# Performance work log

Measured on AMD Instinct MI355X. Metric: run time of the kernel, lower is better.

## Reference

```python
import jax, jax.numpy as jnp
import numpy as np

N_NODES = 50000
N_EDGES = 1_600_000
IN_FEAT = 64
HIDDEN = 64
OUT_FEAT = 10
NUM_LAYERS = 8
ALPHA = 0.1
THETA = 0.5
LN_EPS = 1e-5


def setup_inputs() -> dict:
    key = jax.random.key(0)
    ks = jax.random.split(key, 6)
    N, E, Fin, H, C = N_NODES, N_EDGES, IN_FEAT, HIDDEN, OUT_FEAT
    return {
        "x": jax.random.normal(ks[0], (N, Fin), jnp.float32),
        "W_lin": jax.random.normal(ks[1], (Fin, H), jnp.float32) / np.float32(np.sqrt(Fin)),
        "b_lin": jnp.zeros((H,), jnp.float32),
        "Ws": jax.random.normal(ks[2], (NUM_LAYERS, H, H), jnp.float32) / np.float32(np.sqrt(H)),
        "W1": jax.random.normal(ks[3], (2 * H, H), jnp.float32) / np.float32(np.sqrt(2 * H)),
        "b1": jnp.zeros((H,), jnp.float32),
        "ln_g": jnp.ones((H,), jnp.float32),
        "ln_b": jnp.zeros((H,), jnp.float32),
        "W2": jax.random.normal(ks[4], (H, C), jnp.float32) / np.float32(np.sqrt(H)),
        "b2": jnp.zeros((C,), jnp.float32),
        "edge_index": jax.random.randint(ks[5], (2, E), 0, N, jnp.int32),
    }


def _gcn_norm(edge_index, n):
    # PyG gcn_norm: add self-loops, symmetric D^-1/2 A D^-1/2 normalization.
    loop = jnp.arange(n, dtype=edge_index.dtype)
    row = jnp.concatenate([edge_index[0], loop])
    col = jnp.concatenate([edge_index[1], loop])
    w = jnp.ones(row.shape[0], jnp.float32)
    deg = jax.ops.segment_sum(w, col, num_segments=n)
    dinv = jnp.where(deg > 0, jax.lax.rsqrt(deg), 0.0)
    return row, col, dinv[row] * dinv[col]


def reference(x, W_lin, b_lin, Ws, W1, b1, ln_g, ln_b, W2, b2, edge_index):
    n = x.shape[0]
    row, col, vals = _gcn_norm(edge_index, n)
    h = jax.nn.relu(x @ W_lin + b_lin)  # [N, H]
    h0 = h
    for layer in range(NUM_LAYERS):
        beta = np.float32(np.log(THETA / (layer + 1) + 1.0))
        # SpMM: out[i] = sum over edges (i<-j) vals * h[j]
        agg = jax.ops.segment_sum(vals[:, None] * h[col], row, num_segments=n)
        mix = (1.0 - ALPHA) * agg + ALPHA * h0  # GCN2 initial-residual
        h = jax.nn.relu((1.0 - beta) * mix + beta * (mix @ Ws[layer]))  # identity mapping
    # mix_node_features 'cat': gather endpoint features per edge -> [E, 2H]
    line_x = jnp.concatenate([h[edge_index[0]], h[edge_index[1]]], axis=-1)
    # ClassifierMLP2: Linear -> LayerNorm -> ReLU -> Linear
    z = line_x @ W1 + b1
    mu = jnp.mean(z, axis=-1, keepdims=True)
    var = jnp.var(z, axis=-1, keepdims=True)
    z = (z - mu) * jax.lax.rsqrt(var + LN_EPS) * ln_g + ln_b
    z = jax.nn.relu(z)
    return z @ W2 + b2  # [E, out_features]
```

## Files before the change

kernel.cpp:

```cpp
#include <hip/hip_runtime.h>
#include <hip/hip_fp16.h>
#include <math.h>

#define N_NODES 50000
#define N_EDGES 1600000
#define EDGE_GRID 2048
#define ESTRIDE (EDGE_GRID*64)
#define CAP 128

#define NB 64
#define BRANGE 782
#define BCAP 28672
#define BIN_BLOCKS 512
#define EPB (N_EDGES/BIN_BLOCKS)
#define CURPAD 32

using half8  = __attribute__((ext_vector_type(8))) _Float16;
using half4  = __attribute__((ext_vector_type(4))) _Float16;
using float4v = __attribute__((ext_vector_type(4))) float;

__device__ __forceinline__ float rl(float v, int srclane){
  return __int_as_float(__builtin_amdgcn_readlane(__float_as_int(v), srclane));
}

__global__ __launch_bounds__(256) void k_bin(const int* __restrict__ rowE, const int* __restrict__ colE,
                                             unsigned* __restrict__ rstream, unsigned short* __restrict__ cstream,
                                             int* __restrict__ rcur, int* __restrict__ ccur){
  __shared__ int hr[NB], hc[NB], br[NB], bc[NB];
  int t = threadIdx.x;
  if(t < NB){ hr[t] = 0; hc[t] = 0; }
  __syncthreads();
  int e0 = blockIdx.x * EPB;
  for(int e = e0 + t; e < e0 + EPB; e += 256){
    int r = __builtin_nontemporal_load(rowE + e);
    int c = __builtin_nontemporal_load(colE + e);
    atomicAdd(&hr[r/BRANGE], 1);
    atomicAdd(&hc[c/BRANGE], 1);
  }
  __syncthreads();
  if(t < NB){
    br[t] = atomicAdd(&rcur[t*CURPAD], hr[t]); hr[t] = 0;
    bc[t] = atomicAdd(&ccur[t*CURPAD], hc[t]); hc[t] = 0;
  }
  __syncthreads();
  for(int e = e0 + t; e < e0 + EPB; e += 256){
    int r = rowE[e];
    int c = colE[e];
    int rb = r/BRANGE, cb = c/BRANGE;
    int rp = br[rb] + atomicAdd(&hr[rb], 1);
    int cp = bc[cb] + atomicAdd(&hc[cb], 1);
    if(rp < BCAP) rstream[(size_t)rb*BCAP + rp] = ((unsigned)r << 16) | (unsigned)c;
    if(cp < BCAP) cstream[(size_t)cb*BCAP + cp] = (unsigned short)c;
  }
}

__global__ __launch_bounds__(256) void k_build(const unsigned* __restrict__ rstream,
                                               const unsigned short* __restrict__ cstream,
                                               const int* __restrict__ rcur, const int* __restrict__ ccur,
                                               int* __restrict__ row_fill, int* __restrict__ degcnt,
                                               unsigned short* __restrict__ csr_col){
  __shared__ int lf[BRANGE];
  int b = blockIdx.x & (NB-1);
  int role = blockIdx.x >> 6;
  int base = b*BRANGE;
  int range = min(BRANGE, N_NODES - base);
  int t = threadIdx.x;
  for(int i=t;i<range;i+=256) lf[i] = 0;
  __syncthreads();
  if(role == 0){
    int cnt = min(rcur[b*CURPAD], BCAP);
    const unsigned* sp = rstream + (size_t)b*BCAP;
    for(int i=t;i<cnt;i+=256){
      unsigned rc = sp[i];
      int r = (int)(rc >> 16), c = (int)(rc & 0xffffu);
      int pos = atomicAdd(&lf[r-base], 1);
      if(pos < CAP) csr_col[(size_t)r*CAP + pos] = (unsigned short)c;
    }
    __syncthreads();
    for(int i=t;i<range;i+=256) row_fill[base+i] = lf[i];
  } else {
    int cnt = min(ccur[b*CURPAD], BCAP);
    const unsigned short* sp = cstream + (size_t)b*BCAP;
    for(int i=t;i<cnt;i+=256){
      int c = (int)sp[i];
      atomicAdd(&lf[c-base], 1);
    }
    __syncthreads();
    for(int i=t;i<range;i+=256) degcnt[base+i] = lf[i];
  }
}

__global__ void k_dinv(int* __restrict__ degcnt_rdeg, float* __restrict__ dinv,
                       __half* __restrict__ gA, __half* __restrict__ gB){
  int i = blockIdx.x*256 + threadIdx.x;
  if(i < N_NODES){
    float dp1 = (float)(degcnt_rdeg[i] + 1);
    dinv[i] = rsqrtf(dp1);
    ((float*)degcnt_rdeg)[i] = sqrtf(dp1);
  }
  if(i < 64){
    gA[(size_t)N_NODES*64 + i] = __float2half(0.f);
    gB[(size_t)N_NODES*64 + i] = __float2half(0.f);
  }
}


__global__ __launch_bounds__(256) void k_lin0(const float* __restrict__ x, const float* __restrict__ W,
                                              const float* __restrict__ b, const float* __restrict__ dinv,
                                              __half* __restrict__ h0, __half* __restrict__ g0){
  __shared__ float Wl[4096];
  int t = threadIdx.x;
  for(int i=t;i<4096;i+=256) Wl[i] = W[i];
  __syncthreads();
  int wave = t>>6, lane = t&63;
  int row0 = blockIdx.x*16 + wave*4;
  float4 xq = ((const float4*)(x + (size_t)row0*64))[lane];
  float a0=0,a1=0,a2=0,a3=0;
  #pragma unroll
  for(int k=0;k<64;k++){
    float w = Wl[k*64+lane];
    float comp = ((k&3)==0)?xq.x:((k&3)==1)?xq.y:((k&3)==2)?xq.z:xq.w;
    a0 += rl(comp,      (k>>2)) * w;
    a1 += rl(comp, 16 + (k>>2)) * w;
    a2 += rl(comp, 32 + (k>>2)) * w;
    a3 += rl(comp, 48 + (k>>2)) * w;
  }
  float bb = b[lane];
  float h[4] = {fmaxf(a0+bb,0.f), fmaxf(a1+bb,0.f), fmaxf(a2+bb,0.f), fmaxf(a3+bb,0.f)};
  #pragma unroll
  for(int r=0;r<4;r++){
    float dv = dinv[row0+r];
    h0[(size_t)(row0+r)*64+lane] = __float2half(h[r]);
    g0[(size_t)(row0+r)*64+lane] = __float2half(dv*h[r]);
  }
}

__global__ __launch_bounds__(256) void k_ab(const __half* __restrict__ g, const float* __restrict__ rdeg,
                                            const float* __restrict__ W1,
                                            __half* __restrict__ A, __half* __restrict__ B){
  __shared__ float Wa[4096];
  __shared__ float Wb[4096];
  int t = threadIdx.x;
  for(int i=t;i<4096;i+=256){ Wa[i] = W1[i]; Wb[i] = W1[4096+i]; }
  __syncthreads();
  int wave = t>>6, lane = t&63;
  int row0 = blockIdx.x*16 + wave*4;
  int myrow = row0 + (lane>>4);
  float rd = rdeg[myrow];
  const __half2* hp = (const __half2*)(g + (size_t)row0*64);
  __half2 p01 = hp[2*lane], p23 = hp[2*lane+1];
  float2 f01 = __half22float2(p01), f23 = __half22float2(p23);
  float4 xq = make_float4(f01.x*rd, f01.y*rd, f23.x*rd, f23.y*rd);
  float a0=0,a1=0,a2=0,a3=0,b0=0,b1=0,b2=0,b3=0;
  #pragma unroll
  for(int k=0;k<64;k++){
    float wa = Wa[k*64+lane], wb = Wb[k*64+lane];
    float comp = ((k&3)==0)?xq.x:((k&3)==1)?xq.y:((k&3)==2)?xq.z:xq.w;
    float s0 = rl(comp,      (k>>2));
    float s1 = rl(comp, 16 + (k>>2));
    float s2 = rl(comp, 32 + (k>>2));
    float s3 = rl(comp, 48 + (k>>2));
    a0 += s0*wa; a1 += s1*wa; a2 += s2*wa; a3 += s3*wa;
    b0 += s0*wb; b1 += s1*wb; b2 += s2*wb; b3 += s3*wb;
  }
  A[(size_t)(row0+0)*64+lane]=__float2half(a0); A[(size_t)(row0+1)*64+lane]=__float2half(a1);
  A[(size_t)(row0+2)*64+lane]=__float2half(a2); A[(size_t)(row0+3)*64+lane]=__float2half(a3);
  B[(size_t)(row0+0)*64+lane]=__float2half(b0); B[(size_t)(row0+1)*64+lane]=__float2half(b1);
  B[(size_t)(row0+2)*64+lane]=__float2half(b2); B[(size_t)(row0+3)*64+lane]=__float2half(b3);
}

__global__ __launch_bounds__(256) void k_layer(const __half* __restrict__ g_in, const __half* __restrict__ h0,
                          const int* __restrict__ row_fill, const unsigned short* __restrict__ csr_col,
                          const float* __restrict__ dinv,
                          const float* __restrict__ Wsl, float beta, __half* __restrict__ g_out){
  __shared__ __align__(16) _Float16 tile[16*72];
  int t = threadIdx.x, wave = t>>6, lane = t&63;
  int quad = lane>>4, l15 = lane&15;

  half8 bfrag0, bfrag1;
  int n = 16*wave + l15;
  #pragma unroll
  for(int j=0;j<8;j++){
    int k0 = quad*8 + j;
    int k1 = 32 + quad*8 + j;
    float v0 = beta*Wsl[k0*64+n] + ((k0==n)?(1.f-beta):0.f);
    float v1 = beta*Wsl[k1*64+n] + ((k1==n)?(1.f-beta):0.f);
    bfrag0[j] = (_Float16)v0;
    bfrag1[j] = (_Float16)v1;
  }

  int i0 = blockIdx.x*16;
  int iw = i0 + 4*wave;

  int deg[4], cv[4];
  half4 selfv[4], h0v[4];
  float dv[4];
  #pragma unroll
  for(int r=0;r<4;r++) deg[r] = min(row_fill[iw+r], CAP);
  #pragma unroll
  for(int r=0;r<4;r++){
    const unsigned short* colp = csr_col + (size_t)(iw+r)*CAP;
    cv[r] = (lane < deg[r]) ? (int)__builtin_nontemporal_load(colp + lane) : 0;
  }
  #pragma unroll
  for(int r=0;r<4;r++){
    dv[r]    = dinv[iw+r];
    selfv[r] = *(const half4*)(g_in + (size_t)(iw+r)*64 + 4*l15);
    h0v[r]   = *(const half4*)(h0   + (size_t)(iw+r)*64 + 4*l15);
  }

  for(int r=0;r<4;r++){
    const unsigned short* colp = csr_col + (size_t)(iw+r)*CAP;
    float4v acc = {0.f,0.f,0.f,0.f};
    int base = 0;
    int cur  = cv[r];
    for(;;){
      int rem = deg[r] - base; if(rem > 64) rem = 64;
      int nit = (rem + 3) >> 2;
      int it = 0;
      for(; it+4<=nit; it+=4){
        int i0x = 4*it + quad, i1x = i0x+4, i2x = i0x+8, i3x = i0x+12;
        int c0 = __shfl(cur, i0x, 64); c0 = (i0x < rem) ? c0 : N_NODES;
        int c1 = __shfl(cur, i1x, 64); c1 = (i1x < rem) ? c1 : N_NODES;
        int c2 = __shfl(cur, i2x, 64); c2 = (i2x < rem) ? c2 : N_NODES;
        int c3 = __shfl(cur, i3x, 64); c3 = (i3x < rem) ? c3 : N_NODES;
        half4 v0 = *(const half4*)(g_in + (size_t)c0*64 + 4*l15);
        half4 v1 = *(const half4*)(g_in + (size_t)c1*64 + 4*l15);
        half4 v2 = *(const half4*)(g_in + (size_t)c2*64 + 4*l15);
        half4 v3 = *(const half4*)(g_in + (size_t)c3*64 + 4*l15);
        #pragma unroll
        for(int k=0;k<4;k++) acc[k] += ((float)v0[k]+(float)v1[k]) + ((float)v2[k]+(float)v3[k]);
      }
      for(; it+2<=nit; it+=2){
        int i0x = 4*it + quad, i1x = i0x+4;
        int c0 = __shfl(cur, i0x, 64); c0 = (i0x < rem) ? c0 : N_NODES;
        int c1 = __shfl(cur, i1x, 64); c1 = (i1x < rem) ? c1 : N_NODES;
        half4 v0 = *(const half4*)(g_in + (size_t)c0*64 + 4*l15);
        half4 v1 = *(const half4*)(g_in + (size_t)c1*64 + 4*l15);
        #pragma unroll
        for(int k=0;k<4;k++) acc[k] += (float)v0[k] + (float)v1[k];
      }
      if(it < nit){
        int i0x = 4*it + quad;
        int c0 = __shfl(cur, i0x, 64); c0 = (i0x < rem) ? c0 : N_NODES;
        half4 v0 = *(const half4*)(g_in + (size_t)c0*64 + 4*l15);
        #pragma unroll
        for(int k=0;k<4;k++) acc[k] += (float)v0[k];
      }
      base += 64;
      if(base >= deg[r]) break;
      cur = (base + lane < deg[r]) ? (int)__builtin_nontemporal_load(colp + base + lane) : 0;
    }
    #pragma unroll
    for(int k=0;k<4;k++){
      acc[k] += __shfl_xor(acc[k], 16, 64);
      acc[k] += __shfl_xor(acc[k], 32, 64);
    }
    if(quad == 0){
      half4 mixv;
      #pragma unroll
      for(int k=0;k<4;k++){
        float m = 0.9f*dv[r]*(acc[k] + (float)selfv[r][k]) + 0.1f*(float)h0v[r][k];
        mixv[k] = (_Float16)m;
      }
      *(half4*)&tile[(4*wave+r)*72 + 4*l15] = mixv;
    }
  }
  __syncthreads();

  float4v acc4 = {0.f,0.f,0.f,0.f};
  half8 afrag0 = *(const half8*)&tile[l15*72 + quad*8];
  half8 afrag1 = *(const half8*)&tile[l15*72 + quad*8 + 32];
  acc4 = __builtin_amdgcn_mfma_f32_16x16x32_f16(afrag0, bfrag0, acc4, 0,0,0);
  acc4 = __builtin_amdgcn_mfma_f32_16x16x32_f16(afrag1, bfrag1, acc4, 0,0,0);
  #pragma unroll
  for(int r=0;r<4;r++){
    int row = quad*4 + r;
    float dvo = dinv[i0+row];
    g_out[(size_t)(i0+row)*64 + n] = __float2half(dvo*fmaxf(acc4[r], 0.f));
  }
}

__global__ __launch_bounds__(256) void k_edge(const __half* __restrict__ A, const __half* __restrict__ B,
                         const int* __restrict__ srcE, const int* __restrict__ dstE,
                         const float* __restrict__ b1v, const float* __restrict__ lng,
                         const float* __restrict__ lnb, const float* __restrict__ W2,
                         const float* __restrict__ b2v, float* __restrict__ out){
  int t = threadIdx.x, wave = t>>6, lane = t&63;
  int l15 = lane&15, quad = lane>>4;

  half8 bf0, bf1;
  #pragma unroll
  for(int j=0;j<8;j++){
    float w0 = (l15<10) ? W2[(quad*8+j)*10 + l15]    : 0.f;
    float w1 = (l15<10) ? W2[(32+quad*8+j)*10 + l15] : 0.f;
    bf0[j] = (_Float16)w0;
    bf1[j] = (_Float16)w1;
  }
  float b1r0[8], b1r1[8], gr0[8], gr1[8], br0[8], br1[8];
  #pragma unroll
  for(int j=0;j<8;j++){
    b1r0[j] = b1v[quad*8+j];    b1r1[j] = b1v[32+quad*8+j];
    gr0[j]  = lng[quad*8+j];    gr1[j]  = lng[32+quad*8+j];
    br0[j]  = lnb[quad*8+j];    br1[j]  = lnb[32+quad*8+j];
  }
  float bias = (l15<10) ? b2v[l15] : 0.f;

  int eb0 = blockIdx.x*64 + wave*16;
  int sC = __builtin_nontemporal_load(srcE + eb0 + l15);
  int dC = __builtin_nontemporal_load(dstE + eb0 + l15);
  int sN = 0, dN = 0;
  if(eb0 + ESTRIDE < N_EDGES){
    sN = __builtin_nontemporal_load(srcE + eb0 + ESTRIDE + l15);
    dN = __builtin_nontemporal_load(dstE + eb0 + ESTRIDE + l15);
  }
  half8 A0 = *(const half8*)(A + (size_t)sC*64 + quad*8);
  half8 A1 = *(const half8*)(A + (size_t)sC*64 + 32 + quad*8);
  half8 G0 = *(const half8*)(B + (size_t)dC*64 + quad*8);
  half8 G1 = *(const half8*)(B + (size_t)dC*64 + 32 + quad*8);

  for(int eb = eb0; eb < N_EDGES; eb += ESTRIDE){
    int s2 = 0, d2 = 0;
    if(eb + 2*ESTRIDE < N_EDGES){
      s2 = __builtin_nontemporal_load(srcE + eb + 2*ESTRIDE + l15);
      d2 = __builtin_nontemporal_load(dstE + eb + 2*ESTRIDE + l15);
    }
    half8 nA0 = *(const half8*)(A + (size_t)sN*64 + quad*8);
    half8 nA1 = *(const half8*)(A + (size_t)sN*64 + 32 + quad*8);
    half8 nG0 = *(const half8*)(B + (size_t)dN*64 + quad*8);
    half8 nG1 = *(const half8*)(B + (size_t)dN*64 + 32 + quad*8);

    float z0[8], z1[8];
    float s1 = 0.f, s2acc = 0.f;
    #pragma unroll
    for(int j=0;j<8;j++){
      float za = (float)A0[j] + (float)G0[j] + b1r0[j];
      float zb = (float)A1[j] + (float)G1[j] + b1r1[j];
      z0[j]=za; z1[j]=zb;
      s1 += za + zb;
      s2acc += za*za + zb*zb;
    }
    s1 += __shfl_xor(s1,16,64); s1 += __shfl_xor(s1,32,64);
    s2acc += __shfl_xor(s2acc,16,64); s2acc += __shfl_xor(s2acc,32,64);
    float mu  = s1*(1.f/64.f);
    float var = s2acc*(1.f/64.f) - mu*mu;
    float rs  = rsqrtf(var + 1e-5f);
    half8 af0, af1;
    #pragma unroll
    for(int j=0;j<8;j++){
      af0[j] = (_Float16)fmaxf((z0[j]-mu)*rs*gr0[j] + br0[j], 0.f);
      af1[j] = (_Float16)fmaxf((z1[j]-mu)*rs*gr1[j] + br1[j], 0.f);
    }
    float4v acc = {0.f,0.f,0.f,0.f};
    acc = __builtin_amdgcn_mfma_f32_16x16x32_f16(af0, bf0, acc, 0,0,0);
    acc = __builtin_amdgcn_mfma_f32_16x16x32_f16(af1, bf1, acc, 0,0,0);
    if(l15 < 10){
      #pragma unroll
      for(int r=0;r<4;r++){
        __builtin_nontemporal_store(acc[r] + bias, &out[(size_t)(eb + quad*4 + r)*10 + l15]);
      }
    }
    A0=nA0; A1=nA1; G0=nG0; G1=nG1;
    sN=s2; dN=d2;
  }
}


extern "C" void kernel_launch(void* const* d_in, const int* in_sizes, int n_in,
                              void* d_out, int out_size, void* d_ws, size_t ws_size,
                              hipStream_t stream){
  const float* x     = (const float*)d_in[0];
  const float* W_lin = (const float*)d_in[1];
  const float* b_lin = (const float*)d_in[2];
  const float* Ws    = (const float*)d_in[3];
  const float* W1    = (const float*)d_in[4];
  const float* b1    = (const float*)d_in[5];
  const float* ln_g  = (const float*)d_in[6];
  const float* ln_b  = (const float*)d_in[7];
  const float* W2    = (const float*)d_in[8];
  const float* b2    = (const float*)d_in[9];
  const int*   eidx  = (const int*)d_in[10];
  const int*   rowE  = eidx;
  const int*   colE  = eidx + N_EDGES;
  float* out = (float*)d_out;

  char* ws = (char*)d_ws;
  size_t o = 0;
  auto alloc = [&](size_t bytes)->char*{ char* p = ws + o; o = (o + bytes + 255) & ~(size_t)255; return p; };
  int*   row_fill= (int*)  alloc((size_t)N_NODES*4);
  int*   degcnt  = (int*)  alloc((size_t)N_NODES*4);
  float* dinv    = (float*)alloc((size_t)N_NODES*4);
  unsigned short* csr_col = (unsigned short*)alloc((size_t)N_NODES*CAP*2);
  unsigned* rstream = (unsigned*)alloc((size_t)NB*BCAP*4);
  unsigned short* cstream = (unsigned short*)alloc((size_t)NB*BCAP*2);
  int*   rcur    = (int*)  alloc((size_t)NB*CURPAD*4);
  int*   ccur    = (int*)  alloc((size_t)NB*CURPAD*4);
  __half* h0     = (__half*)alloc((size_t)(N_NODES+1)*64*2);
  __half* gA     = (__half*)alloc((size_t)(N_NODES+1)*64*2);
  __half* gB     = (__half*)alloc((size_t)(N_NODES+1)*64*2);
  float* rdeg    = (float*)degcnt;

  hipMemsetAsync(rcur, 0, (size_t)NB*CURPAD*4, stream);
  hipMemsetAsync(ccur, 0, (size_t)NB*CURPAD*4, stream);

  k_bin  <<<BIN_BLOCKS, 256, 0, stream>>>(rowE, colE, rstream, cstream, rcur, ccur);
  k_build<<<2*NB, 256, 0, stream>>>(rstream, cstream, rcur, ccur, row_fill, degcnt, csr_col);
  k_dinv <<<(N_NODES+255)/256, 256, 0, stream>>>(degcnt, dinv, gA, gB);

  k_lin0<<<N_NODES/16, 256, 0, stream>>>(x, W_lin, b_lin, dinv, h0, gA);

  const __half* gin = gA;
  __half* bufs[2] = {gB, gA};
  for(int L=0; L<8; L++){
    float beta = logf(0.5f/(float)(L+1) + 1.0f);
    __half* gout = bufs[L&1];
    k_layer<<<(N_NODES+15)/16, 256, 0, stream>>>(gin, h0, row_fill, csr_col, dinv,
                                                 Ws + (size_t)L*4096, beta, gout);
    gin = gout;
  }
  __half* Abuf = gB;
  __half* Bbuf = h0;
  k_ab<<<N_NODES/16, 256, 0, stream>>>(gA, rdeg, W1, Abuf, Bbuf);
  k_edge<<<EDGE_GRID, 256, 0, stream>>>(Abuf, Bbuf, rowE, colE, b1, ln_g, ln_b, W2, b2, out);
}
```

Before: 503.9 us.

## Gather neighbor rows with 16-byte loads in SpMM and drop edge-kernel prefetch

The layer SpMM now has each lane gather 8 halves (16 bytes) per neighbor. Eight lanes cover one 64-wide row, so a wave processes 8 neighbors at a time instead of 4 with 8-byte loads, and one extra xor-shuffle stage completes the reduction. The edge classifier kernel drops its software-pipelined prefetch of the next indices and features and becomes a simple grid-stride loop. The gather change aims to cut load instruction count per byte; removing the prefetch may expose gather latency or may lower register pressure and raise occupancy.

```diff
diff --git a/kernel.cpp b/kernel.cpp
--- a/kernel.cpp
+++ b/kernel.cpp
@@ -5,7 +5,6 @@
 #define N_NODES 50000
 #define N_EDGES 1600000
 #define EDGE_GRID 2048
-#define ESTRIDE (EDGE_GRID*64)
 #define CAP 128
 
 #define NB 64
@@ -176,6 +175,7 @@
   __shared__ __align__(16) _Float16 tile[16*72];
   int t = threadIdx.x, wave = t>>6, lane = t&63;
   int quad = lane>>4, l15 = lane&15;
+  int grp = lane>>3, l8 = lane&7;
 
   half8 bfrag0, bfrag1;
   int n = 16*wave + l15;
@@ -193,7 +193,7 @@
   int iw = i0 + 4*wave;
 
   int deg[4], cv[4];
-  half4 selfv[4], h0v[4];
+  half8 selfv[4], h0v[4];
   float dv[4];
   #pragma unroll
   for(int r=0;r<4;r++) deg[r] = min(row_fill[iw+r], CAP);
@@ -205,65 +205,53 @@
   #pragma unroll
   for(int r=0;r<4;r++){
     dv[r]    = dinv[iw+r];
-    selfv[r] = *(const half4*)(g_in + (size_t)(iw+r)*64 + 4*l15);
-    h0v[r]   = *(const half4*)(h0   + (size_t)(iw+r)*64 + 4*l15);
+    selfv[r] = *(const half8*)(g_in + (size_t)(iw+r)*64 + 8*l8);
+    h0v[r]   = *(const half8*)(h0   + (size_t)(iw+r)*64 + 8*l8);
   }
 
   for(int r=0;r<4;r++){
     const unsigned short* colp = csr_col + (size_t)(iw+r)*CAP;
-    float4v acc = {0.f,0.f,0.f,0.f};
+    float acc[8] = {0,0,0,0,0,0,0,0};
     int base = 0;
     int cur  = cv[r];
     for(;;){
       int rem = deg[r] - base; if(rem > 64) rem = 64;
-      int nit = (rem + 3) >> 2;
+      int nit = (rem + 7) >> 3;
       int it = 0;
-      for(; it+4<=nit; it+=4){
-        int i0x = 4*it + quad, i1x = i0x+4, i2x = i0x+8, i3x = i0x+12;
-        int c0 = __shfl(cur, i0x, 64); c0 = (i0x < rem) ? c0 : N_NODES;
-        int c1 = __shfl(cur, i1x, 64); c1 = (i1x < rem) ? c1 : N_NODES;
-        int c2 = __shfl(cur, i2x, 64); c2 = (i2x < rem) ? c2 : N_NODES;
-        int c3 = __shfl(cur, i3x, 64); c3 = (i3x < rem) ? c3 : N_NODES;
-        half4 v0 = *(const half4*)(g_in + (size_t)c0*64 + 4*l15);
-        half4 v1 = *(const half4*)(g_in + (size_t)c1*64 + 4*l15);
-        half4 v2 = *(const half4*)(g_in + (size_t)c2*64 + 4*l15);
-        half4 v3 = *(const half4*)(g_in + (size_t)c3*64 + 4*l15);
+      for(; it+2<=nit; it+=2){
+        int iA = 8*it + grp, iB = iA + 8;
+        int cA = __shfl(cur, iA, 64); cA = (iA < rem) ? cA : N_NODES;
+        int cB = __shfl(cur, iB, 64); cB = (iB < rem) ? cB : N_NODES;
+        half8 vA = *(const half8*)(g_in + (size_t)cA*64 + 8*l8);
+        half8 vB = *(const half8*)(g_in + (size_t)cB*64 + 8*l8);
         #pragma unroll
-        for(int k=0;k<4;k++) acc[k] += ((float)v0[k]+(float)v1[k]) + ((float)v2[k]+(float)v3[k]);
-      }
-      for(; it+2<=nit; it+=2){
-        int i0x = 4*it + quad, i1x = i0x+4;
-        int c0 = __shfl(cur, i0x, 64); c0 = (i0x < rem) ? c0 : N_NODES;
-        int c1 = __shfl(cur, i1x, 64); c1 = (i1x < rem) ? c1 : N_NODES;
-        half4 v0 = *(const half4*)(g_in + (size_t)c0*64 + 4*l15);
-        half4 v1 = *(const half4*)(g_in + (size_t)c1*64 + 4*l15);
-        #pragma unroll
-        for(int k=0;k<4;k++) acc[k] += (float)v0[k] + (float)v1[k];
+        for(int k=0;k<8;k++) acc[k] += (float)vA[k] + (float)vB[k];
       }
       if(it < nit){
-        int i0x = 4*it + quad;
-        int c0 = __shfl(cur, i0x, 64); c0 = (i0x < rem) ? c0 : N_NODES;
-        half4 v0 = *(const half4*)(g_in + (size_t)c0*64 + 4*l15);
+        int iA = 8*it + grp;
+        int cA = __shfl(cur, iA, 64); cA = (iA < rem) ? cA : N_NODES;
+        half8 vA = *(const half8*)(g_in + (size_t)cA*64 + 8*l8);
         #pragma unroll
-        for(int k=0;k<4;k++) acc[k] += (float)v0[k];
+        for(int k=0;k<8;k++) acc[k] += (float)vA[k];
       }
       base += 64;
       if(base >= deg[r]) break;
       cur = (base + lane < deg[r]) ? (int)__builtin_nontemporal_load(colp + base + lane) : 0;
     }
     #pragma unroll
-    for(int k=0;k<4;k++){
+    for(int k=0;k<8;k++){
+      acc[k] += __shfl_xor(acc[k], 8, 64);
       acc[k] += __shfl_xor(acc[k], 16, 64);
       acc[k] += __shfl_xor(acc[k], 32, 64);
     }
-    if(quad == 0){
-      half4 mixv;
+    if(grp == 0){
+      half8 mixv;
       #pragma unroll
-      for(int k=0;k<4;k++){
+      for(int k=0;k<8;k++){
         float m = 0.9f*dv[r]*(acc[k] + (float)selfv[r][k]) + 0.1f*(float)h0v[r][k];
         mixv[k] = (_Float16)m;
       }
-      *(half4*)&tile[(4*wave+r)*72 + 4*l15] = mixv;
+      *(half8*)&tile[(4*wave+r)*72 + 8*l8] = mixv;
     }
   }
   __syncthreads();
@@ -306,44 +294,28 @@
   }
   float bias = (l15<10) ? b2v[l15] : 0.f;
 
-  int eb0 = blockIdx.x*64 + wave*16;
-  int sC = __builtin_nontemporal_load(srcE + eb0 + l15);
-  int dC = __builtin_nontemporal_load(dstE + eb0 + l15);
-  int sN = 0, dN = 0;
-  if(eb0 + ESTRIDE < N_EDGES){
-    sN = __builtin_nontemporal_load(srcE + eb0 + ESTRIDE + l15);
-    dN = __builtin_nontemporal_load(dstE + eb0 + ESTRIDE + l15);
-  }
-  half8 A0 = *(const half8*)(A + (size_t)sC*64 + quad*8);
-  half8 A1 = *(const half8*)(A + (size_t)sC*64 + 32 + quad*8);
-  half8 G0 = *(const half8*)(B + (size_t)dC*64 + quad*8);
-  half8 G1 = *(const half8*)(B + (size_t)dC*64 + 32 + quad*8);
-
-  for(int eb = eb0; eb < N_EDGES; eb += ESTRIDE){
-    int s2 = 0, d2 = 0;
-    if(eb + 2*ESTRIDE < N_EDGES){
-      s2 = __builtin_nontemporal_load(srcE + eb + 2*ESTRIDE + l15);
-      d2 = __builtin_nontemporal_load(dstE + eb + 2*ESTRIDE + l15);
-    }
-    half8 nA0 = *(const half8*)(A + (size_t)sN*64 + quad*8);
-    half8 nA1 = *(const half8*)(A + (size_t)sN*64 + 32 + quad*8);
-    half8 nG0 = *(const half8*)(B + (size_t)dN*64 + quad*8);
-    half8 nG1 = *(const half8*)(B + (size_t)dN*64 + 32 + quad*8);
-
+  for(int eb = blockIdx.x*64 + wave*16; eb < N_EDGES; eb += EDGE_GRID*64){
+    int e = eb + l15;
+    int s = __builtin_nontemporal_load(srcE + e);
+    int d = __builtin_nontemporal_load(dstE + e);
+    half8 a0 = *(const half8*)(A + (size_t)s*64 + quad*8);
+    half8 a1 = *(const half8*)(A + (size_t)s*64 + 32 + quad*8);
+    half8 g0 = *(const half8*)(B + (size_t)d*64 + quad*8);
+    half8 g1 = *(const half8*)(B + (size_t)d*64 + 32 + quad*8);
     float z0[8], z1[8];
-    float s1 = 0.f, s2acc = 0.f;
+    float s1 = 0.f, s2 = 0.f;
     #pragma unroll
     for(int j=0;j<8;j++){
-      float za = (float)A0[j] + (float)G0[j] + b1r0[j];
-      float zb = (float)A1[j] + (float)G1[j] + b1r1[j];
+      float za = (float)a0[j] + (float)g0[j] + b1r0[j];
+      float zb = (float)a1[j] + (float)g1[j] + b1r1[j];
       z0[j]=za; z1[j]=zb;
       s1 += za + zb;
-      s2acc += za*za + zb*zb;
+      s2 += za*za + zb*zb;
     }
     s1 += __shfl_xor(s1,16,64); s1 += __shfl_xor(s1,32,64);
-    s2acc += __shfl_xor(s2acc,16,64); s2acc += __shfl_xor(s2acc,32,64);
+    s2 += __shfl_xor(s2,16,64); s2 += __shfl_xor(s2,32,64);
     float mu  = s1*(1.f/64.f);
-    float var = s2acc*(1.f/64.f) - mu*mu;
+    float var = s2*(1.f/64.f) - mu*mu;
     float rs  = rsqrtf(var + 1e-5f);
     half8 af0, af1;
     #pragma unroll
@@ -360,8 +332,6 @@
         __builtin_nontemporal_store(acc[r] + bias, &out[(size_t)(eb + quad*4 + r)*10 + l15]);
       }
     }
-    A0=nA0; A1=nA1; G0=nG0; G1=nG1;
-    sN=s2; dN=d2;
   }
 }
 
```

Result: slower. 550.6 us (+9.3%).

## Process edges in row-bucketed order in edge kernel for gather locality

Applied to the files above, without the earlier changes.

The bin pass now stores the original edge index alongside row/col in a 64-bit record. The final edge kernel walks these row-bucketed records instead of the raw edge list, so source-row gathers stay within one node range and hit cache better. Output is scattered back using the stored edge id. The cost is wider stream records, scattered output stores, and dropping the software prefetch pipeline from the old loop.

```diff
diff --git a/kernel.cpp b/kernel.cpp
--- a/kernel.cpp
+++ b/kernel.cpp
@@ -5,7 +5,6 @@
 #define N_NODES 50000
 #define N_EDGES 1600000
 #define EDGE_GRID 2048
-#define ESTRIDE (EDGE_GRID*64)
 #define CAP 128
 
 #define NB 64
@@ -24,7 +23,8 @@
 }
 
 __global__ __launch_bounds__(256) void k_bin(const int* __restrict__ rowE, const int* __restrict__ colE,
-                                             unsigned* __restrict__ rstream, unsigned short* __restrict__ cstream,
+                                             unsigned long long* __restrict__ rstream,
+                                             unsigned short* __restrict__ cstream,
                                              int* __restrict__ rcur, int* __restrict__ ccur){
   __shared__ int hr[NB], hc[NB], br[NB], bc[NB];
   int t = threadIdx.x;
@@ -49,12 +49,13 @@
     int rb = r/BRANGE, cb = c/BRANGE;
     int rp = br[rb] + atomicAdd(&hr[rb], 1);
     int cp = bc[cb] + atomicAdd(&hc[cb], 1);
-    if(rp < BCAP) rstream[(size_t)rb*BCAP + rp] = ((unsigned)r << 16) | (unsigned)c;
+    if(rp < BCAP) rstream[(size_t)rb*BCAP + rp] =
+        ((unsigned long long)(unsigned)e << 32) | ((unsigned)r << 16) | (unsigned)c;
     if(cp < BCAP) cstream[(size_t)cb*BCAP + cp] = (unsigned short)c;
   }
 }
 
-__global__ __launch_bounds__(256) void k_build(const unsigned* __restrict__ rstream,
+__global__ __launch_bounds__(256) void k_build(const unsigned long long* __restrict__ rstream,
                                                const unsigned short* __restrict__ cstream,
                                                const int* __restrict__ rcur, const int* __restrict__ ccur,
                                                int* __restrict__ row_fill, int* __restrict__ degcnt,
@@ -69,10 +70,10 @@
   __syncthreads();
   if(role == 0){
     int cnt = min(rcur[b*CURPAD], BCAP);
-    const unsigned* sp = rstream + (size_t)b*BCAP;
+    const unsigned long long* sp = rstream + (size_t)b*BCAP;
     for(int i=t;i<cnt;i+=256){
-      unsigned rc = sp[i];
-      int r = (int)(rc >> 16), c = (int)(rc & 0xffffu);
+      unsigned long long rec = sp[i];
+      int r = (int)((rec >> 16) & 0xffffu), c = (int)(rec & 0xffffu);
       int pos = atomicAdd(&lf[r-base], 1);
       if(pos < CAP) csr_col[(size_t)r*CAP + pos] = (unsigned short)c;
     }
@@ -183,10 +184,8 @@
   for(int j=0;j<8;j++){
     int k0 = quad*8 + j;
     int k1 = 32 + quad*8 + j;
-    float v0 = beta*Wsl[k0*64+n] + ((k0==n)?(1.f-beta):0.f);
-    float v1 = beta*Wsl[k1*64+n] + ((k1==n)?(1.f-beta):0.f);
-    bfrag0[j] = (_Float16)v0;
-    bfrag1[j] = (_Float16)v1;
+    bfrag0[j] = (_Float16)(beta*Wsl[k0*64+n] + ((k0==n)?(1.f-beta):0.f));
+    bfrag1[j] = (_Float16)(beta*Wsl[k1*64+n] + ((k1==n)?(1.f-beta):0.f));
   }
 
   int i0 = blockIdx.x*16;
@@ -282,7 +281,7 @@
 }
 
 __global__ __launch_bounds__(256) void k_edge(const __half* __restrict__ A, const __half* __restrict__ B,
-                         const int* __restrict__ srcE, const int* __restrict__ dstE,
+                         const unsigned long long* __restrict__ rstream, const int* __restrict__ rcur,
                          const float* __restrict__ b1v, const float* __restrict__ lng,
                          const float* __restrict__ lnb, const float* __restrict__ W2,
                          const float* __restrict__ b2v, float* __restrict__ out){
@@ -306,44 +305,39 @@
   }
   float bias = (l15<10) ? b2v[l15] : 0.f;
 
-  int eb0 = blockIdx.x*64 + wave*16;
-  int sC = __builtin_nontemporal_load(srcE + eb0 + l15);
-  int dC = __builtin_nontemporal_load(dstE + eb0 + l15);
-  int sN = 0, dN = 0;
-  if(eb0 + ESTRIDE < N_EDGES){
-    sN = __builtin_nontemporal_load(srcE + eb0 + ESTRIDE + l15);
-    dN = __builtin_nontemporal_load(dstE + eb0 + ESTRIDE + l15);
-  }
-  half8 A0 = *(const half8*)(A + (size_t)sC*64 + quad*8);
-  half8 A1 = *(const half8*)(A + (size_t)sC*64 + 32 + quad*8);
-  half8 G0 = *(const half8*)(B + (size_t)dC*64 + quad*8);
-  half8 G1 = *(const half8*)(B + (size_t)dC*64 + 32 + quad*8);
-
-  for(int eb = eb0; eb < N_EDGES; eb += ESTRIDE){
-    int s2 = 0, d2 = 0;
-    if(eb + 2*ESTRIDE < N_EDGES){
-      s2 = __builtin_nontemporal_load(srcE + eb + 2*ESTRIDE + l15);
-      d2 = __builtin_nontemporal_load(dstE + eb + 2*ESTRIDE + l15);
-    }
-    half8 nA0 = *(const half8*)(A + (size_t)sN*64 + quad*8);
-    half8 nA1 = *(const half8*)(A + (size_t)sN*64 + 32 + quad*8);
-    half8 nG0 = *(const half8*)(B + (size_t)dN*64 + quad*8);
-    half8 nG1 = *(const half8*)(B + (size_t)dN*64 + 32 + quad*8);
-
+  int bid = blockIdx.x;
+  int bucket = ((bid & 7) << 3) | ((bid >> 3) & 7);
+  int sub = bid >> 6;
+  int cnt = rcur[bucket*CURPAD]; if(cnt > BCAP) cnt = BCAP;
+  const unsigned long long* sp = rstream + (size_t)bucket*BCAP;
+  int chunk = ((cnt + 2047) >> 11) << 6;
+  int start = sub*chunk;
+  int end = start + chunk; if(end > cnt) end = cnt;
+
+  for(int eo = start + wave*16; eo < end; eo += 64){
+    int idx = eo + l15; if(idx >= end) idx = end - 1;
+    unsigned long long rec = sp[idx];
+    int s = (int)((rec >> 16) & 0xffffu);
+    int d = (int)(rec & 0xffffu);
+    int e = (int)(rec >> 32);
+    half8 a0 = *(const half8*)(A + (size_t)s*64 + quad*8);
+    half8 a1 = *(const half8*)(A + (size_t)s*64 + 32 + quad*8);
+    half8 g0 = *(const half8*)(B + (size_t)d*64 + quad*8);
+    half8 g1 = *(const half8*)(B + (size_t)d*64 + 32 + quad*8);
     float z0[8], z1[8];
-    float s1 = 0.f, s2acc = 0.f;
+    float s1 = 0.f, s2 = 0.f;
     #pragma unroll
     for(int j=0;j<8;j++){
-      float za = (float)A0[j] + (float)G0[j] + b1r0[j];
-      float zb = (float)A1[j] + (float)G1[j] + b1r1[j];
+      float za = (float)a0[j] + (float)g0[j] + b1r0[j];
+      float zb = (float)a1[j] + (float)g1[j] + b1r1[j];
       z0[j]=za; z1[j]=zb;
       s1 += za + zb;
-      s2acc += za*za + zb*zb;
+      s2 += za*za + zb*zb;
     }
     s1 += __shfl_xor(s1,16,64); s1 += __shfl_xor(s1,32,64);
-    s2acc += __shfl_xor(s2acc,16,64); s2acc += __shfl_xor(s2acc,32,64);
+    s2 += __shfl_xor(s2,16,64); s2 += __shfl_xor(s2,32,64);
     float mu  = s1*(1.f/64.f);
-    float var = s2acc*(1.f/64.f) - mu*mu;
+    float var = s2*(1.f/64.f) - mu*mu;
     float rs  = rsqrtf(var + 1e-5f);
     half8 af0, af1;
     #pragma unroll
@@ -354,14 +348,16 @@
     float4v acc = {0.f,0.f,0.f,0.f};
     acc = __builtin_amdgcn_mfma_f32_16x16x32_f16(af0, bf0, acc, 0,0,0);
     acc = __builtin_amdgcn_mfma_f32_16x16x32_f16(af1, bf1, acc, 0,0,0);
+    int esl[4];
+    #pragma unroll
+    for(int r=0;r<4;r++) esl[r] = __shfl(e, quad*4 + r, 64);
     if(l15 < 10){
       #pragma unroll
       for(int r=0;r<4;r++){
-        __builtin_nontemporal_store(acc[r] + bias, &out[(size_t)(eb + quad*4 + r)*10 + l15]);
+        if(eo + quad*4 + r < end)
+          __builtin_nontemporal_store(acc[r] + bias, &out[(size_t)esl[r]*10 + l15]);
       }
     }
-    A0=nA0; A1=nA1; G0=nG0; G1=nG1;
-    sN=s2; dN=d2;
   }
 }
 
@@ -391,7 +387,7 @@
   int*   degcnt  = (int*)  alloc((size_t)N_NODES*4);
   float* dinv    = (float*)alloc((size_t)N_NODES*4);
   unsigned short* csr_col = (unsigned short*)alloc((size_t)N_NODES*CAP*2);
-  unsigned* rstream = (unsigned*)alloc((size_t)NB*BCAP*4);
+  unsigned long long* rstream = (unsigned long long*)alloc((size_t)NB*BCAP*8);
   unsigned short* cstream = (unsigned short*)alloc((size_t)NB*BCAP*2);
   int*   rcur    = (int*)  alloc((size_t)NB*CURPAD*4);
   int*   ccur    = (int*)  alloc((size_t)NB*CURPAD*4);
@@ -421,5 +417,5 @@
   __half* Abuf = gB;
   __half* Bbuf = h0;
   k_ab<<<N_NODES/16, 256, 0, stream>>>(gA, rdeg, W1, Abuf, Bbuf);
-  k_edge<<<EDGE_GRID, 256, 0, stream>>>(Abuf, Bbuf, rowE, colE, b1, ln_g, ln_b, W2, b2, out);
-}
+  k_edge<<<EDGE_GRID, 256, 0, stream>>>(Abuf, Bbuf, rstream, rcur, b1, ln_g, ln_b, W2, b2, out);
+}
```

After: 526.0 us. 1.04x slower.
